# Kernel tuning notes

Hardware: AMD Instinct MI355X
Metric: run time of the kernel (lower is better)

The kernel has to match this reference:

```python
import jax, jax.numpy as jnp
import numpy as np

E, D_IN, D_HID, D_OUT, B = 8, 128, 256, 128, 65536


def setup_inputs() -> dict:
    key = jax.random.key(0)
    ks = jax.random.split(key, 6)
    s1 = 1.0 / np.sqrt(D_IN)
    s2 = 1.0 / np.sqrt(D_HID)
    return {
        "x": jax.random.normal(ks[0], (B, D_IN), dtype=jnp.float32),
        "weights": jax.random.uniform(ks[1], (B, E), dtype=jnp.float32),
        "W1": jax.random.uniform(ks[2], (E, D_IN, D_HID), jnp.float32, -s1, s1),
        "b1": jax.random.uniform(ks[3], (E, D_HID), jnp.float32, -s1, s1),
        "W2": jax.random.uniform(ks[4], (E, D_HID, D_OUT), jnp.float32, -s2, s2),
        "b2": jax.random.uniform(ks[5], (E, D_OUT), jnp.float32, -s2, s2),
    }


def reference(x, weights, W1, b1, W2, b2):
    # all-experts dense MLP: every expert processes the full batch
    h = jax.nn.relu(jnp.einsum("bi,eih->beh", x, W1) + b1[None])  # [B,E,H]
    y = jnp.einsum("beh,eho->beo", h, W2) + b2[None]              # [B,E,O]
    # weighted combine over experts
    return jnp.einsum("beo,be->bo", y, weights)                   # [B,O]
```

## Files before the change

kernel.cpp:

```cpp
#include <hip/hip_runtime.h>


#define E_    8
#define DIN_  128
#define DH_   256
#define DOUT_ 128
#define BM_   256

typedef __attribute__((ext_vector_type(8))) short bf16x8;
typedef __attribute__((ext_vector_type(4))) float f32x4;

__device__ __forceinline__ unsigned short f2bf(float f) {
  union { float f; unsigned int u; } v; v.f = f;
  unsigned int u = v.u;
  u += 0x7fffu + ((u >> 16) & 1u);
  return (unsigned short)(u >> 16);
}

__device__ __forceinline__ void gload_lds16(const void* g, void* l) {
  __builtin_amdgcn_global_load_lds(
      (const __attribute__((address_space(1))) unsigned int*)g,
      (__attribute__((address_space(3))) unsigned int*)l, 16, 0, 0);
}

__global__ __launch_bounds__(256) void transpose_to_bf16(
    const float* __restrict__ in, unsigned short* __restrict__ out,
    int R, int C, int nTR, int nTC)
{
  __shared__ float tile[64][65];
  const int tiles = nTR * nTC;
  const int mat = blockIdx.x / tiles;
  const int tt  = blockIdx.x % tiles;
  const int tr = tt / nTC, tc = tt % nTC;
  const float* src = in + (size_t)mat * R * C;
  unsigned short* dst = out + (size_t)mat * R * C;
  const int tid = threadIdx.x;
  #pragma unroll
  for (int i = 0; i < 16; ++i) {
    int row = i * 4 + (tid >> 6);
    int col = tid & 63;
    tile[row][col] = src[(size_t)(tr * 64 + row) * C + tc * 64 + col];
  }
  __syncthreads();
  #pragma unroll
  for (int i = 0; i < 8; ++i) {
    int c  = i * 8 + (tid >> 5);
    int r0 = (tid & 31) * 2;
    unsigned int pk = (unsigned int)f2bf(tile[r0][c]) |
                      ((unsigned int)f2bf(tile[r0 + 1][c]) << 16);
    *(unsigned int*)(dst + (size_t)(tc * 64 + c) * R + tr * 64 + r0) = pk;
  }
}


__device__ __forceinline__ void stage_chunk(
    const unsigned short* __restrict__ W1t, const unsigned short* __restrict__ W2t,
    unsigned char* buf, int t, int tid, int wv)
{
  const int e = t >> 2, hc = t & 3;
  const unsigned char* w1b =
      (const unsigned char*)(W1t + (size_t)(e * DH_ + hc * 64) * DIN_);
  #pragma unroll
  for (int r = 0; r < 2; ++r) {
    const int o  = (r * 512 + tid) * 16;
    const int c  = o >> 8;
    const int ko = (o & 255) ^ ((c & 7) << 4);
    gload_lds16(w1b + c * 256 + ko, buf + r * 8192 + wv * 1024);
  }
  const unsigned char* w2b = (const unsigned char*)W2t;
  #pragma unroll
  for (int r = 0; r < 2; ++r) {
    const int o  = (r * 512 + tid) * 16;
    const int n  = o >> 7;
    const int co = (o & 127) ^ ((n & 7) << 4);
    gload_lds16(w2b + (size_t)(e * DOUT_ + n) * 512 + hc * 128 + co,
                buf + 16384 + r * 8192 + wv * 1024);
  }
}

__global__ __launch_bounds__(512, 2) void moe_main(
    const float* __restrict__ x, const float* __restrict__ wts,
    const float* __restrict__ b1, const float* __restrict__ b2,
    const unsigned short* __restrict__ W1t, const unsigned short* __restrict__ W2t,
    float* __restrict__ out)
{
  __shared__ __align__(16) unsigned char Wbuf[2][32768];
  __shared__ __align__(16) unsigned char hbuf[32768];
  __shared__ float wls[E_ * BM_];

  const int tid  = threadIdx.x;
  const int lane = tid & 63;
  const int wv   = tid >> 6;
  const int q    = lane >> 4;
  const int l16  = lane & 15;
  const int swz  = (l16 & 7) << 4;
  const long bm  = (long)blockIdx.x * BM_;

  const int m_half = (wv >> 1) * 64;
  const int c_half = (wv & 1) * 32;
  const int n_half = (wv & 1) * 64;

  for (int i = tid; i < E_ * BM_; i += 512) {
    int e = i >> 8, m = i & 255;
    wls[i] = wts[(bm + m) * E_ + e];
  }

  stage_chunk(W1t, W2t, Wbuf[0], 0, tid, wv);

  bf16x8 xf[4][4];
  #pragma unroll
  for (int mf = 0; mf < 4; ++mf) {
    const float* xr = x + (bm + m_half + mf * 16 + l16) * DIN_;
    #pragma unroll
    for (int ks = 0; ks < 4; ++ks) {
      int k0 = ks * 32 + q * 8;
      float4 lo = *(const float4*)(xr + k0);
      float4 hi = *(const float4*)(xr + k0 + 4);
      bf16x8 f;
      f[0] = (short)f2bf(lo.x); f[1] = (short)f2bf(lo.y);
      f[2] = (short)f2bf(lo.z); f[3] = (short)f2bf(lo.w);
      f[4] = (short)f2bf(hi.x); f[5] = (short)f2bf(hi.y);
      f[6] = (short)f2bf(hi.z); f[7] = (short)f2bf(hi.w);
      xf[mf][ks] = f;
    }
  }

  f32x4 oacc[4][4];
  #pragma unroll
  for (int i = 0; i < 4; ++i)
    #pragma unroll
    for (int j = 0; j < 4; ++j) oacc[i][j] = 0.0f;

  for (int t = 0; t < 32; ++t) {
    const int e = t >> 2, hc = t & 3;
    unsigned char* Wc = Wbuf[t & 1];
    __syncthreads();
    if (t + 1 < 32) stage_chunk(W1t, W2t, Wbuf[(t + 1) & 1], t + 1, tid, wv);

    float wreg[4];
    #pragma unroll
    for (int mf = 0; mf < 4; ++mf) wreg[mf] = wls[e * 256 + m_half + mf * 16 + l16];

    f32x4 hacc[2][4];
    #pragma unroll
    for (int i = 0; i < 2; ++i)
      #pragma unroll
      for (int j = 0; j < 4; ++j) hacc[i][j] = 0.0f;

    #pragma unroll
    for (int ks = 0; ks < 4; ++ks) {
      const int kb = ks * 64 + q * 16;
      bf16x8 a0 = *(const bf16x8*)(Wc + (c_half +      l16) * 256 + (kb ^ swz));
      bf16x8 a1 = *(const bf16x8*)(Wc + (c_half + 16 + l16) * 256 + (kb ^ swz));
      #pragma unroll
      for (int mf = 0; mf < 4; ++mf) {
        hacc[0][mf] = __builtin_amdgcn_mfma_f32_16x16x32_bf16(a0, xf[mf][ks], hacc[0][mf], 0, 0, 0);
        hacc[1][mf] = __builtin_amdgcn_mfma_f32_16x16x32_bf16(a1, xf[mf][ks], hacc[1][mf], 0, 0, 0);
      }
    }
    #pragma unroll
    for (int cf = 0; cf < 2; ++cf) {
      const int c0 = c_half + cf * 16 + q * 4;
      float4 bb = *(const float4*)(b1 + e * DH_ + hc * 64 + c0);
      #pragma unroll
      for (int mf = 0; mf < 4; ++mf) {
        const int m = m_half + mf * 16 + l16;
        f32x4 v = hacc[cf][mf];
        const float w = wreg[mf];
        float h0 = fmaxf(v[0] + bb.x, 0.0f) * w;
        float h1 = fmaxf(v[1] + bb.y, 0.0f) * w;
        float h2 = fmaxf(v[2] + bb.z, 0.0f) * w;
        float h3 = fmaxf(v[3] + bb.w, 0.0f) * w;
        uint2 pk;
        pk.x = (unsigned int)f2bf(h0) | ((unsigned int)f2bf(h1) << 16);
        pk.y = (unsigned int)f2bf(h2) | ((unsigned int)f2bf(h3) << 16);
        *(uint2*)(hbuf + m * 128 + ((c0 * 2) ^ swz)) = pk;
      }
    }
    __syncthreads();

    const unsigned char* W2c = Wc + 16384;
    #pragma unroll
    for (int ks = 0; ks < 2; ++ks) {
      const int clb = ks * 64 + q * 16;
      bf16x8 a2[4], bh[4];
      #pragma unroll
      for (int nf = 0; nf < 4; ++nf)
        a2[nf] = *(const bf16x8*)(W2c + (n_half + nf * 16 + l16) * 128 + (clb ^ swz));
      #pragma unroll
      for (int mf = 0; mf < 4; ++mf)
        bh[mf] = *(const bf16x8*)(hbuf + (m_half + mf * 16 + l16) * 128 + (clb ^ swz));
      #pragma unroll
      for (int nf = 0; nf < 4; ++nf)
        #pragma unroll
        for (int mf = 0; mf < 4; ++mf)
          oacc[nf][mf] = __builtin_amdgcn_mfma_f32_16x16x32_bf16(a2[nf], bh[mf], oacc[nf][mf], 0, 0, 0);
    }
  }

  #pragma unroll
  for (int nf = 0; nf < 4; ++nf) {
    const int n0 = n_half + nf * 16 + q * 4;
    #pragma unroll
    for (int mf = 0; mf < 4; ++mf) {
      const int m = m_half + mf * 16 + l16;
      f32x4 v = oacc[nf][mf];
      #pragma unroll
      for (int e = 0; e < E_; ++e) {
        const float w = wls[e * 256 + m];
        float4 bb = *(const float4*)(b2 + e * DOUT_ + n0);
        v[0] += w * bb.x; v[1] += w * bb.y; v[2] += w * bb.z; v[3] += w * bb.w;
      }
      float4 o; o.x = v[0]; o.y = v[1]; o.z = v[2]; o.w = v[3];
      *(float4*)(out + (bm + m) * DOUT_ + n0) = o;
    }
  }
}

extern "C" void kernel_launch(void* const* d_in, const int* in_sizes, int n_in,
                              void* d_out, int out_size, void* d_ws, size_t ws_size,
                              hipStream_t stream) {
  const float* x   = (const float*)d_in[0];
  const float* wts = (const float*)d_in[1];
  const float* W1  = (const float*)d_in[2];
  const float* b1  = (const float*)d_in[3];
  const float* W2  = (const float*)d_in[4];
  const float* b2  = (const float*)d_in[5];
  float* out = (float*)d_out;

  unsigned short* W1t = (unsigned short*)d_ws;
  unsigned short* W2t = W1t + (size_t)E_ * DH_ * DIN_;

  transpose_to_bf16<<<64, 256, 0, stream>>>(W1, W1t, 128, 256, 2, 4);
  transpose_to_bf16<<<64, 256, 0, stream>>>(W2, W2t, 256, 128, 4, 2);

  moe_main<<<65536 / BM_, 512, 0, stream>>>(x, wts, b1, b2, W1t, W2t, out);
}
```

Baseline: 113.9 us.

## Keep hidden activations in registers via 32x32 MFMA and permlane swaps

```diff
diff --git a/kernel.cpp b/kernel.cpp
--- a/kernel.cpp
+++ b/kernel.cpp
@@ -5,16 +5,31 @@
 #define DIN_  128
 #define DH_   256
 #define DOUT_ 128
-#define BM_   256
+#define BM_   128
+#define NCHUNK 32
 
 typedef __attribute__((ext_vector_type(8))) short bf16x8;
-typedef __attribute__((ext_vector_type(4))) float f32x4;
+typedef __attribute__((ext_vector_type(16))) float f32x16;
+typedef __attribute__((ext_vector_type(2))) unsigned int uint2v;
 
 __device__ __forceinline__ unsigned short f2bf(float f) {
   union { float f; unsigned int u; } v; v.f = f;
   unsigned int u = v.u;
   u += 0x7fffu + ((u >> 16) & 1u);
   return (unsigned short)(u >> 16);
+}
+
+__device__ __forceinline__ unsigned int cvt_pk_bf16(float lo, float hi) {
+  unsigned int r;
+  asm("v_cvt_pk_bf16_f32 %0, %1, %2" : "=v"(r) : "v"(lo), "v"(hi));
+  return r;
+}
+
+__device__ __forceinline__ bf16x8 pack4(unsigned int a, unsigned int b,
+                                        unsigned int c, unsigned int d) {
+  union { unsigned int u[4]; bf16x8 v; } t;
+  t.u[0] = a; t.u[1] = b; t.u[2] = c; t.u[3] = d;
+  return t.v;
 }
 
 __device__ __forceinline__ void gload_lds16(const void* g, void* l) {
@@ -52,7 +67,6 @@
   }
 }
 
-
 __device__ __forceinline__ void stage_chunk(
     const unsigned short* __restrict__ W1t, const unsigned short* __restrict__ W2t,
     unsigned char* buf, int t, int tid, int wv)
@@ -61,158 +75,145 @@
   const unsigned char* w1b =
       (const unsigned char*)(W1t + (size_t)(e * DH_ + hc * 64) * DIN_);
   #pragma unroll
-  for (int r = 0; r < 2; ++r) {
-    const int o  = (r * 512 + tid) * 16;
+  for (int r = 0; r < 4; ++r) {
+    const int o  = (r * 256 + tid) * 16;
     const int c  = o >> 8;
     const int ko = (o & 255) ^ ((c & 7) << 4);
-    gload_lds16(w1b + c * 256 + ko, buf + r * 8192 + wv * 1024);
+    gload_lds16(w1b + c * 256 + ko, buf + r * 4096 + wv * 1024);
   }
   const unsigned char* w2b = (const unsigned char*)W2t;
   #pragma unroll
-  for (int r = 0; r < 2; ++r) {
-    const int o  = (r * 512 + tid) * 16;
+  for (int r = 0; r < 4; ++r) {
+    const int o  = (r * 256 + tid) * 16;
     const int n  = o >> 7;
     const int co = (o & 127) ^ ((n & 7) << 4);
     gload_lds16(w2b + (size_t)(e * DOUT_ + n) * 512 + hc * 128 + co,
-                buf + 16384 + r * 8192 + wv * 1024);
-  }
-}
-
-__global__ __launch_bounds__(512, 2) void moe_main(
+                buf + 16384 + r * 4096 + wv * 1024);
+  }
+}
+
+__global__ __launch_bounds__(256, 2) void moe_main(
     const float* __restrict__ x, const float* __restrict__ wts,
     const float* __restrict__ b1, const float* __restrict__ b2,
     const unsigned short* __restrict__ W1t, const unsigned short* __restrict__ W2t,
     float* __restrict__ out)
 {
   __shared__ __align__(16) unsigned char Wbuf[2][32768];
-  __shared__ __align__(16) unsigned char hbuf[32768];
-  __shared__ float wls[E_ * BM_];
 
   const int tid  = threadIdx.x;
   const int lane = tid & 63;
   const int wv   = tid >> 6;
-  const int q    = lane >> 4;
-  const int l16  = lane & 15;
-  const int swz  = (l16 & 7) << 4;
+  const int l32  = lane & 31;
+  const int hi   = lane >> 5;
+  const int swz  = (l32 & 7) << 4;
   const long bm  = (long)blockIdx.x * BM_;
-
-  const int m_half = (wv >> 1) * 64;
-  const int c_half = (wv & 1) * 32;
-  const int n_half = (wv & 1) * 64;
-
-  for (int i = tid; i < E_ * BM_; i += 512) {
-    int e = i >> 8, m = i & 255;
-    wls[i] = wts[(bm + m) * E_ + e];
-  }
+  const int m    = wv * 32 + l32;
 
   stage_chunk(W1t, W2t, Wbuf[0], 0, tid, wv);
 
-  bf16x8 xf[4][4];
-  #pragma unroll
-  for (int mf = 0; mf < 4; ++mf) {
-    const float* xr = x + (bm + m_half + mf * 16 + l16) * DIN_;
+  float wreg[8];
+  {
+    float4 a = *(const float4*)(wts + (bm + m) * E_);
+    float4 b = *(const float4*)(wts + (bm + m) * E_ + 4);
+    wreg[0] = a.x; wreg[1] = a.y; wreg[2] = a.z; wreg[3] = a.w;
+    wreg[4] = b.x; wreg[5] = b.y; wreg[6] = b.z; wreg[7] = b.w;
+  }
+
+  bf16x8 xf[8];
+  #pragma unroll
+  for (int ks = 0; ks < 8; ++ks) {
+    const float* xr = x + (bm + m) * DIN_ + ks * 16 + hi * 8;
+    float4 a = *(const float4*)xr;
+    float4 b = *(const float4*)(xr + 4);
+    xf[ks] = pack4(cvt_pk_bf16(a.x, a.y), cvt_pk_bf16(a.z, a.w),
+                   cvt_pk_bf16(b.x, b.y), cvt_pk_bf16(b.z, b.w));
+  }
+
+  f32x16 oacc[4];
+  #pragma unroll
+  for (int nf = 0; nf < 4; ++nf) oacc[nf] = 0.0f;
+
+  for (int t = 0; t < NCHUNK; ++t) {
+    const int e = t >> 2, hc = t & 3;
+    const unsigned char* Wc = Wbuf[t & 1];
+    __syncthreads();
+
+    float bb[2][16];
+    #pragma unroll
+    for (int cf = 0; cf < 2; ++cf)
+      #pragma unroll
+      for (int g = 0; g < 4; ++g) {
+        float4 b = *(const float4*)(b1 + e * DH_ + hc * 64 + cf * 32 + g * 8 + hi * 4);
+        bb[cf][4 * g + 0] = b.x; bb[cf][4 * g + 1] = b.y;
+        bb[cf][4 * g + 2] = b.z; bb[cf][4 * g + 3] = b.w;
+      }
+
+    if (t + 1 < NCHUNK) stage_chunk(W1t, W2t, Wbuf[(t + 1) & 1], t + 1, tid, wv);
+
+    f32x16 hacc[2];
+    hacc[0] = 0.0f; hacc[1] = 0.0f;
+    #pragma unroll
+    for (int ks = 0; ks < 8; ++ks) {
+      const int kb = ks * 32 + hi * 16;
+      #pragma unroll
+      for (int cf = 0; cf < 2; ++cf) {
+        bf16x8 a = *(const bf16x8*)(Wc + (cf * 32 + l32) * 256 + (kb ^ swz));
+        hacc[cf] = __builtin_amdgcn_mfma_f32_32x32x16_bf16(a, xf[ks], hacc[cf], 0, 0, 0);
+      }
+    }
+
+    const float w = wreg[e];
+    bf16x8 hfr[4];
+    #pragma unroll
+    for (int cf = 0; cf < 2; ++cf) {
+      unsigned int u[8];
+      #pragma unroll
+      for (int p = 0; p < 8; ++p) {
+        float h0 = fmaxf(hacc[cf][2 * p]     + bb[cf][2 * p],     0.0f) * w;
+        float h1 = fmaxf(hacc[cf][2 * p + 1] + bb[cf][2 * p + 1], 0.0f) * w;
+        u[p] = cvt_pk_bf16(h0, h1);
+      }
+      uint2v s02 = __builtin_amdgcn_permlane32_swap(u[0], u[2], false, false);
+      uint2v s13 = __builtin_amdgcn_permlane32_swap(u[1], u[3], false, false);
+      uint2v s46 = __builtin_amdgcn_permlane32_swap(u[4], u[6], false, false);
+      uint2v s57 = __builtin_amdgcn_permlane32_swap(u[5], u[7], false, false);
+      hfr[2 * cf]     = pack4(s02[0], s13[0], s02[1], s13[1]);
+      hfr[2 * cf + 1] = pack4(s46[0], s57[0], s46[1], s57[1]);
+    }
+
     #pragma unroll
     for (int ks = 0; ks < 4; ++ks) {
-      int k0 = ks * 32 + q * 8;
-      float4 lo = *(const float4*)(xr + k0);
-      float4 hi = *(const float4*)(xr + k0 + 4);
-      bf16x8 f;
-      f[0] = (short)f2bf(lo.x); f[1] = (short)f2bf(lo.y);
-      f[2] = (short)f2bf(lo.z); f[3] = (short)f2bf(lo.w);
-      f[4] = (short)f2bf(hi.x); f[5] = (short)f2bf(hi.y);
-      f[6] = (short)f2bf(hi.z); f[7] = (short)f2bf(hi.w);
-      xf[mf][ks] = f;
-    }
-  }
-
-  f32x4 oacc[4][4];
-  #pragma unroll
-  for (int i = 0; i < 4; ++i)
-    #pragma unroll
-    for (int j = 0; j < 4; ++j) oacc[i][j] = 0.0f;
-
-  for (int t = 0; t < 32; ++t) {
-    const int e = t >> 2, hc = t & 3;
-    unsigned char* Wc = Wbuf[t & 1];
-    __syncthreads();
-    if (t + 1 < 32) stage_chunk(W1t, W2t, Wbuf[(t + 1) & 1], t + 1, tid, wv);
-
-    float wreg[4];
-    #pragma unroll
-    for (int mf = 0; mf < 4; ++mf) wreg[mf] = wls[e * 256 + m_half + mf * 16 + l16];
-
-    f32x4 hacc[2][4];
-    #pragma unroll
-    for (int i = 0; i < 2; ++i)
-      #pragma unroll
-      for (int j = 0; j < 4; ++j) hacc[i][j] = 0.0f;
-
-    #pragma unroll
-    for (int ks = 0; ks < 4; ++ks) {
-      const int kb = ks * 64 + q * 16;
-      bf16x8 a0 = *(const bf16x8*)(Wc + (c_half +      l16) * 256 + (kb ^ swz));
-      bf16x8 a1 = *(const bf16x8*)(Wc + (c_half + 16 + l16) * 256 + (kb ^ swz));
-      #pragma unroll
-      for (int mf = 0; mf < 4; ++mf) {
-        hacc[0][mf] = __builtin_amdgcn_mfma_f32_16x16x32_bf16(a0, xf[mf][ks], hacc[0][mf], 0, 0, 0);
-        hacc[1][mf] = __builtin_amdgcn_mfma_f32_16x16x32_bf16(a1, xf[mf][ks], hacc[1][mf], 0, 0, 0);
-      }
-    }
-    #pragma unroll
-    for (int cf = 0; cf < 2; ++cf) {
-      const int c0 = c_half + cf * 16 + q * 4;
-      float4 bb = *(const float4*)(b1 + e * DH_ + hc * 64 + c0);
-      #pragma unroll
-      for (int mf = 0; mf < 4; ++mf) {
-        const int m = m_half + mf * 16 + l16;
-        f32x4 v = hacc[cf][mf];
-        const float w = wreg[mf];
-        float h0 = fmaxf(v[0] + bb.x, 0.0f) * w;
-        float h1 = fmaxf(v[1] + bb.y, 0.0f) * w;
-        float h2 = fmaxf(v[2] + bb.z, 0.0f) * w;
-        float h3 = fmaxf(v[3] + bb.w, 0.0f) * w;
-        uint2 pk;
-        pk.x = (unsigned int)f2bf(h0) | ((unsigned int)f2bf(h1) << 16);
-        pk.y = (unsigned int)f2bf(h2) | ((unsigned int)f2bf(h3) << 16);
-        *(uint2*)(hbuf + m * 128 + ((c0 * 2) ^ swz)) = pk;
-      }
-    }
-    __syncthreads();
-
-    const unsigned char* W2c = Wc + 16384;
-    #pragma unroll
-    for (int ks = 0; ks < 2; ++ks) {
-      const int clb = ks * 64 + q * 16;
-      bf16x8 a2[4], bh[4];
-      #pragma unroll
-      for (int nf = 0; nf < 4; ++nf)
-        a2[nf] = *(const bf16x8*)(W2c + (n_half + nf * 16 + l16) * 128 + (clb ^ swz));
-      #pragma unroll
-      for (int mf = 0; mf < 4; ++mf)
-        bh[mf] = *(const bf16x8*)(hbuf + (m_half + mf * 16 + l16) * 128 + (clb ^ swz));
-      #pragma unroll
-      for (int nf = 0; nf < 4; ++nf)
-        #pragma unroll
-        for (int mf = 0; mf < 4; ++mf)
-          oacc[nf][mf] = __builtin_amdgcn_mfma_f32_16x16x32_bf16(a2[nf], bh[mf], oacc[nf][mf], 0, 0, 0);
-    }
-  }
-
+      const int cb = ks * 32 + hi * 16;
+      #pragma unroll
+      for (int nf = 0; nf < 4; ++nf) {
+        bf16x8 b = *(const bf16x8*)(Wc + 16384 + (nf * 32 + l32) * 128 + (cb ^ swz));
+        oacc[nf] = __builtin_amdgcn_mfma_f32_32x32x16_bf16(hfr[ks], b, oacc[nf], 0, 0, 0);
+      }
+    }
+  }
+
+  const unsigned int z = 0;
+  bf16x8 wfrag = pack4(hi ? z : cvt_pk_bf16(wreg[0], wreg[1]),
+                       hi ? z : cvt_pk_bf16(wreg[2], wreg[3]),
+                       hi ? z : cvt_pk_bf16(wreg[4], wreg[5]),
+                       hi ? z : cvt_pk_bf16(wreg[6], wreg[7]));
   #pragma unroll
   for (int nf = 0; nf < 4; ++nf) {
-    const int n0 = n_half + nf * 16 + q * 4;
-    #pragma unroll
-    for (int mf = 0; mf < 4; ++mf) {
-      const int m = m_half + mf * 16 + l16;
-      f32x4 v = oacc[nf][mf];
-      #pragma unroll
-      for (int e = 0; e < E_; ++e) {
-        const float w = wls[e * 256 + m];
-        float4 bb = *(const float4*)(b2 + e * DOUT_ + n0);
-        v[0] += w * bb.x; v[1] += w * bb.y; v[2] += w * bb.z; v[3] += w * bb.w;
-      }
-      float4 o; o.x = v[0]; o.y = v[1]; o.z = v[2]; o.w = v[3];
-      *(float4*)(out + (bm + m) * DOUT_ + n0) = o;
+    const float* bp = b2 + nf * 32 + l32;
+    bf16x8 bfrag = pack4(
+        hi ? z : cvt_pk_bf16(bp[0 * DOUT_], bp[1 * DOUT_]),
+        hi ? z : cvt_pk_bf16(bp[2 * DOUT_], bp[3 * DOUT_]),
+        hi ? z : cvt_pk_bf16(bp[4 * DOUT_], bp[5 * DOUT_]),
+        hi ? z : cvt_pk_bf16(bp[6 * DOUT_], bp[7 * DOUT_]));
+    oacc[nf] = __builtin_amdgcn_mfma_f32_32x32x16_bf16(wfrag, bfrag, oacc[nf], 0, 0, 0);
+  }
+
+  #pragma unroll
+  for (int nf = 0; nf < 4; ++nf) {
+    #pragma unroll
+    for (int r = 0; r < 16; ++r) {
+      const int mloc = (r & 3) + 8 * (r >> 2) + 4 * hi;
+      out[(bm + wv * 32 + mloc) * DOUT_ + nf * 32 + l32] = oacc[nf][r];
     }
   }
 }
@@ -234,5 +235,5 @@
   transpose_to_bf16<<<64, 256, 0, stream>>>(W1, W1t, 128, 256, 2, 4);
   transpose_to_bf16<<<64, 256, 0, stream>>>(W2, W2t, 256, 128, 4, 2);
 
-  moe_main<<<65536 / BM_, 512, 0, stream>>>(x, wts, b1, b2, W1t, W2t, out);
-}
+  moe_main<<<65536 / BM_, 256, 0, stream>>>(x, wts, b1, b2, W1t, W2t, out);
+}
```

Result: faster. 93.82 us (-17.6%).
